# Kernel tuning notes

Hardware: AMD Instinct MI355X
Metric: run time of the kernel (lower is better)

## Reference

```python
import jax, jax.numpy as jnp
import numpy as np

N = 2048      # num_nodes
B = 16        # batch
D_IN = 2      # input_dim per node
UNITS = 64    # rnn_units
F = D_IN + UNITS   # concat feature size = 66
M = 3         # num_matrices = (1 support + 1 adp hop)*K(=1) + 1 identity
E = N * 16    # sparse support edges (avg degree 16)


def _spmm(rows, cols, vals, x):
    # sparse support @ x, x: (N, K); equivalent of torch.sparse.mm
    return jax.ops.segment_sum(vals[:, None] * x[cols], rows, num_segments=N)


def _gconv(inputs, state, W, support_rows, support_cols, support_vals, adp):
    # inputs: (B, N*D_IN), state: (B, N*units) -> out: (B, N*out_dim)
    x = jnp.concatenate([inputs.reshape(B, N, -1), state.reshape(B, N, -1)], axis=2)  # (B,N,F)
    f = x.shape[2]
    x0 = x.transpose(1, 2, 0).reshape(N, f * B)                # (N, F*B)
    # diffusion step 1 over the single random_walk support
    x1 = _spmm(support_rows, support_cols, support_vals, x0)   # (N, F*B)
    # adaptive adjacency, k_hop=1 -> adp_lst = [adp], applied to x0
    x_temp = x0.reshape(N, f, B).transpose(2, 0, 1)            # (B,N,F)
    x2 = jnp.einsum('bnm,bmf->bnf', adp, x_temp)               # (B,N,F)
    x2 = x2.transpose(1, 2, 0).reshape(N, f * B)
    xs = jnp.stack([x0, x1, x2], axis=0)                       # (M,N,F*B)
    xs = xs.reshape(M, N, f, B).transpose(3, 1, 2, 0).reshape(B * N, f * M)
    out = xs @ W                                               # (B*N, out_dim)  (no bias: source never adds it)
    return out.reshape(B, N * W.shape[1])


def setup_inputs() -> dict:
    key = jax.random.key(0)
    ks = jax.random.split(key, 8)
    inputs = jax.random.normal(ks[0], (B, N * D_IN), dtype=jnp.float32)
    hx = jax.random.normal(ks[1], (B, N * UNITS), dtype=jnp.float32)
    adp = jax.random.uniform(ks[2], (B, N, N), dtype=jnp.float32) / N  # ~row-stochastic adaptive adj
    support_rows = jax.random.randint(ks[3], (E,), 0, N, dtype=jnp.int32)
    support_cols = jax.random.randint(ks[4], (E,), 0, N, dtype=jnp.int32)
    support_vals = jax.random.uniform(ks[5], (E,), dtype=jnp.float32) / 16.0
    W_ru = jax.random.normal(ks[6], (F * M, 2 * UNITS), dtype=jnp.float32) * 0.05
    W_c = jax.random.normal(ks[7], (F * M, UNITS), dtype=jnp.float32) * 0.05
    return dict(inputs=inputs, hx=hx, adp=adp, support_rows=support_rows,
                support_cols=support_cols, support_vals=support_vals,
                W_ru=W_ru, W_c=W_c, time_axis=0)


def reference(inputs, hx, adp, support_rows, support_cols, support_vals, W_ru, W_c, time_axis):
    # GRU with graph convolution gates (use_gc_for_ru=True, activation=tanh)
    ru = jax.nn.sigmoid(_gconv(inputs, hx, W_ru, support_rows, support_cols, support_vals, adp))
    ru = ru.reshape(B, N, 2 * UNITS)
    r = ru[..., :UNITS].reshape(B, N * UNITS)
    u = ru[..., UNITS:].reshape(B, N * UNITS)
    c = jnp.tanh(_gconv(inputs, r * hx, W_c, support_rows, support_cols, support_vals, adp))
    return u * hx + (1.0 - u) * c
```

## Files before the change

kernel.cpp:

```cpp
#include <hip/hip_runtime.h>
#include <cstdint>
#include <cstddef>

#define DN 2048
#define DB 16
#define DE 32768
#define FPAD 96

typedef __bf16 bf16x8 __attribute__((ext_vector_type(8)));
typedef float f32x4 __attribute__((ext_vector_type(4)));

__global__ __launch_bounds__(256) void prep_kernel(
    const float* __restrict__ inputs, const float* __restrict__ hx,
    const float* __restrict__ Wru, const float* __restrict__ Wc,
    __bf16* __restrict__ xcat1, __bf16* __restrict__ xcat2,
    __bf16* __restrict__ wtru, __bf16* __restrict__ wtc,
    int* __restrict__ cnt) {
  int idx = blockIdx.x * 256 + threadIdx.x;
  const int T1 = DB * DN * FPAD;
  if (idx < 2 * T1) {
    int which = idx >= T1 ? 1 : 0;
    int i = idx - which * T1;
    int f = i % FPAD;
    int bn = i / FPAD;
    int n = bn & (DN - 1);
    int b = bn >> 11;
    __bf16 v = (__bf16)0.0f;
    if (f < 2) v = (__bf16)inputs[(b << 12) + n * 2 + f];
    else if (f < 66 && !which) v = (__bf16)hx[((size_t)b << 17) + (n << 6) + (f - 2)];
    if (which) xcat2[i] = v; else xcat1[i] = v;
  } else {
    int j = idx - 2 * T1;
    if (j < 384 * FPAD) {
      int k = j % FPAD, o = j / FPAD;
      wtru[j] = (k < 66) ? (__bf16)Wru[(k * 3 + (o >> 7)) * 128 + (o & 127)] : (__bf16)0.0f;
    } else {
      j -= 384 * FPAD;
      if (j < 192 * FPAD) {
        int k = j % FPAD, o = j / FPAD;
        wtc[j] = (k < 66) ? (__bf16)Wc[(k * 3 + (o >> 6)) * 64 + (o & 63)] : (__bf16)0.0f;
      } else {
        j -= 192 * FPAD;
        if (j < DN) cnt[j] = 0;
      }
    }
  }
}

__global__ __launch_bounds__(512) void csr_count(const int* __restrict__ rows,
                                                 int* __restrict__ cnt) {
  int e = blockIdx.x * 512 + threadIdx.x;
  atomicAdd(&cnt[rows[e]], 1);
}

__global__ __launch_bounds__(1024) void csr_scan(const int* __restrict__ cnt,
                                                 int* __restrict__ csr_ptr,
                                                 int* __restrict__ off) {
  __shared__ int sa[DN];
  __shared__ int sb[DN];
  int t = threadIdx.x;
  int c0 = cnt[t], c1 = cnt[t + 1024];
  sa[t] = c0; sa[t + 1024] = c1;
  __syncthreads();
  int* src = sa; int* dst = sb;
  for (int o = 1; o < DN; o <<= 1) {
    for (int i = t; i < DN; i += 1024) {
      int v = src[i];
      if (i >= o) v += src[i - o];
      dst[i] = v;
    }
    __syncthreads();
    int* tmp = src; src = dst; dst = tmp;
  }
  int e0 = src[t] - c0;
  int e1 = src[t + 1024] - c1;
  csr_ptr[t] = e0; csr_ptr[t + 1024] = e1;
  off[t] = e0; off[t + 1024] = e1;
  if (t == 0) csr_ptr[DN] = DE;
}

__global__ __launch_bounds__(512) void csr_scatter(
    const int* __restrict__ rows, const int* __restrict__ cols,
    const float* __restrict__ vals, int* __restrict__ off,
    int* __restrict__ csr_col, float* __restrict__ csr_val) {
  int e = blockIdx.x * 512 + threadIdx.x;
  int r = rows[e];
  int p = atomicAdd(&off[r], 1);
  csr_col[p] = cols[e];
  csr_val[p] = vals[e];
}

template <int OD>
__global__ __launch_bounds__(256) void small_gemm(
    const __bf16* __restrict__ A, const __bf16* __restrict__ Bt,
    float* __restrict__ Y0, __bf16* __restrict__ y1b, __bf16* __restrict__ y2b) {
  __shared__ __attribute__((aligned(16))) __bf16 As[128 * 104];
  __shared__ __attribute__((aligned(16))) __bf16 Bs[64 * 104];
  int tid = threadIdx.x;
  int wave = tid >> 6, lane = tid & 63;
  int lrow = lane & 15, quad = lane >> 4;
  int r0 = blockIdx.x * 128;
  int c0 = blockIdx.y * 64;
  const uint4* gA = (const uint4*)(A + (size_t)r0 * FPAD);
  const uint4* gB = (const uint4*)(Bt + (size_t)c0 * FPAD);
  uint4* sA = (uint4*)As;
  uint4* sB = (uint4*)Bs;
#pragma unroll
  for (int i = 0; i < 6; ++i) {
    int s = i * 256 + tid;
    int r = s / 12, c4 = s % 12;
    sA[r * 13 + c4] = gA[r * 12 + c4];
  }
#pragma unroll
  for (int i = 0; i < 3; ++i) {
    int s = i * 256 + tid;
    int r = s / 12, c4 = s % 12;
    sB[r * 13 + c4] = gB[r * 12 + c4];
  }
  __syncthreads();
  int wm = wave >> 1, wn = wave & 1;
  f32x4 acc[4][2];
#pragma unroll
  for (int mt = 0; mt < 4; ++mt)
#pragma unroll
    for (int nt = 0; nt < 2; ++nt) acc[mt][nt] = (f32x4){0.f, 0.f, 0.f, 0.f};
#pragma unroll
  for (int kk = 0; kk < 3; ++kk) {
    bf16x8 af[4], bv[2];
#pragma unroll
    for (int mt = 0; mt < 4; ++mt)
      af[mt] = *(const bf16x8*)(As + (wm * 64 + mt * 16 + lrow) * 104 + kk * 32 + quad * 8);
#pragma unroll
    for (int nt = 0; nt < 2; ++nt)
      bv[nt] = *(const bf16x8*)(Bs + (wn * 32 + nt * 16 + lrow) * 104 + kk * 32 + quad * 8);
#pragma unroll
    for (int mt = 0; mt < 4; ++mt)
#pragma unroll
      for (int nt = 0; nt < 2; ++nt)
        acc[mt][nt] = __builtin_amdgcn_mfma_f32_16x16x32_bf16(af[mt], bv[nt], acc[mt][nt], 0, 0, 0);
  }
#pragma unroll
  for (int mt = 0; mt < 4; ++mt)
#pragma unroll
    for (int nt = 0; nt < 2; ++nt)
#pragma unroll
      for (int r = 0; r < 4; ++r) {
        int row = r0 + wm * 64 + mt * 16 + quad * 4 + r;
        int col = c0 + wn * 32 + nt * 16 + lrow;
        float v = acc[mt][nt][r];
        int g = col >> ((OD == 128) ? 7 : 6);
        int oo = col & (OD - 1);
        size_t oi = (size_t)row * OD + oo;
        if (g == 0) Y0[oi] = v;
        else if (g == 1) y1b[oi] = (__bf16)v;
        else y2b[oi] = (__bf16)v;
      }
}

template <int OD>
__global__ __launch_bounds__(256) void gather_pre(
    float* __restrict__ Y0, const __bf16* __restrict__ y1b,
    const int* __restrict__ csr_ptr, const int* __restrict__ csr_col,
    const float* __restrict__ csr_val) {
  constexpr int SH = (OD == 128) ? 7 : 6;
  int idx = blockIdx.x * 256 + threadIdx.x;
  int o = idx & (OD - 1);
  int bn = idx >> SH;
  int n = bn & (DN - 1);
  int b = bn >> 11;
  float acc = Y0[idx];
  int e1 = csr_ptr[n + 1];
  const __bf16* yb = y1b + ((size_t)b << 11) * OD;
  for (int e = csr_ptr[n]; e < e1; ++e)
    acc += csr_val[e] * (float)yb[(size_t)csr_col[e] * OD + o];
  Y0[idx] = acc;
}

template <int OD>
__global__ void transpose_y2(const __bf16* __restrict__ y2b, __bf16* __restrict__ y2t) {
  __shared__ __bf16 tile[32][33];
  int b = blockIdx.z;
  int mb = blockIdx.x * 32, ob = blockIdx.y * 32;
  int tx = threadIdx.x, ty = threadIdx.y;
#pragma unroll
  for (int i = 0; i < 4; ++i)
    tile[ty + i * 8][tx] = y2b[(size_t)(b * DN + mb + ty + i * 8) * OD + ob + tx];
  __syncthreads();
#pragma unroll
  for (int i = 0; i < 4; ++i)
    y2t[(size_t)(b * OD + ob + ty + i * 8) * DN + mb + tx] = tile[tx][ty + i * 8];
}

template <int OD, bool IS_RU>
__global__ __launch_bounds__(256, 4) void adp_gemm(
    const float* __restrict__ adp, const __bf16* __restrict__ y2t,
    const float* __restrict__ pre, const float* __restrict__ hx,
    float* __restrict__ u_buf, __bf16* __restrict__ xcat2,
    float* __restrict__ outp) {
  constexpr int BM = 32;
  constexpr int NT = OD / 32;
  constexpr int LDK = 72;
  constexpr int ASZ = BM * LDK;
  __shared__ __attribute__((aligned(16))) __bf16 As[2 * ASZ];
  int tid = threadIdx.x;
  int wave = tid >> 6, lane = tid & 63;
  int lrow = lane & 15, quad = lane >> 4;
  int hw = blockIdx.x;
  int swz = (hw & 7) * 128 + (hw >> 3);
  int b = swz >> 6;
  int row0 = (swz & 63) * BM;
  const float* Ab = adp + ((size_t)b * DN + row0) * DN;
  const __bf16* Bb = y2t + (size_t)b * OD * (size_t)DN;
  int wm = wave >> 1, wn = wave & 1;
  f32x4 acc[NT];
#pragma unroll
  for (int nt = 0; nt < NT; ++nt) acc[nt] = (f32x4){0.f, 0.f, 0.f, 0.f};

  int ar = tid >> 3;
  int ac = (tid & 7) * 8;
  const float* ap = Ab + (size_t)ar * DN + ac;
  int awofs = ar * LDK + ac;
  int arofs = (wm * 16 + lrow) * LDK;

  f32x4 raA0 = *(const f32x4*)ap;
  f32x4 raA1 = *(const f32x4*)(ap + 4);
  f32x4 raB0 = *(const f32x4*)(ap + 64);
  f32x4 raB1 = *(const f32x4*)(ap + 68);

#pragma unroll 1
  for (int c2 = 0; c2 < DN / 128; ++c2) {
    {
      int c = 2 * c2;
      bf16x8 cv;
#pragma unroll
      for (int j = 0; j < 4; ++j) { cv[j] = (__bf16)raA0[j]; cv[4 + j] = (__bf16)raA1[j]; }
      *(bf16x8*)(As + awofs) = cv;
      bf16x8 bv[2][NT];
#pragma unroll
      for (int kk = 0; kk < 2; ++kk)
#pragma unroll
        for (int nt = 0; nt < NT; ++nt) {
          int rb = wn * (NT * 16) + nt * 16 + lrow;
          bv[kk][nt] = *(const bf16x8*)(Bb + (size_t)rb * DN + c * 64 + (kk * 4 + quad) * 8);
        }
      if (c + 2 < DN / 64) {
        const float* pn = ap + (c + 2) * 64;
        raA0 = *(const f32x4*)pn;
        raA1 = *(const f32x4*)(pn + 4);
      }
      __syncthreads();
#pragma unroll
      for (int kk = 0; kk < 2; ++kk) {
        bf16x8 af = *(const bf16x8*)(As + arofs + (kk * 4 + quad) * 8);
#pragma unroll
        for (int nt = 0; nt < NT; ++nt)
          acc[nt] = __builtin_amdgcn_mfma_f32_16x16x32_bf16(af, bv[kk][nt], acc[nt], 0, 0, 0);
      }
    }
    {
      int c = 2 * c2 + 1;
      bf16x8 cv;
#pragma unroll
      for (int j = 0; j < 4; ++j) { cv[j] = (__bf16)raB0[j]; cv[4 + j] = (__bf16)raB1[j]; }
      *(bf16x8*)(As + ASZ + awofs) = cv;
      bf16x8 bv[2][NT];
#pragma unroll
      for (int kk = 0; kk < 2; ++kk)
#pragma unroll
        for (int nt = 0; nt < NT; ++nt) {
          int rb = wn * (NT * 16) + nt * 16 + lrow;
          bv[kk][nt] = *(const bf16x8*)(Bb + (size_t)rb * DN + c * 64 + (kk * 4 + quad) * 8);
        }
      if (c + 2 < DN / 64) {
        const float* pn = ap + (c + 2) * 64;
        raB0 = *(const f32x4*)pn;
        raB1 = *(const f32x4*)(pn + 4);
      }
      __syncthreads();
#pragma unroll
      for (int kk = 0; kk < 2; ++kk) {
        bf16x8 af = *(const bf16x8*)(As + ASZ + arofs + (kk * 4 + quad) * 8);
#pragma unroll
        for (int nt = 0; nt < NT; ++nt)
          acc[nt] = __builtin_amdgcn_mfma_f32_16x16x32_bf16(af, bv[kk][nt], acc[nt], 0, 0, 0);
      }
    }
  }
#pragma unroll
  for (int nt = 0; nt < NT; ++nt)
#pragma unroll
    for (int r = 0; r < 4; ++r) {
      int n = row0 + wm * 16 + quad * 4 + r;
      int o = wn * (NT * 16) + nt * 16 + lrow;
      float g = acc[nt][r] + pre[((size_t)b * DN + n) * OD + o];
      if (IS_RU) {
        float s = 1.f / (1.f + __expf(-g));
        if (o < 64) {
          float hxv = hx[((size_t)b << 17) + n * 64 + o];
          xcat2[((size_t)b * DN + n) * FPAD + 2 + o] = (__bf16)(s * hxv);
        } else {
          u_buf[((size_t)b * DN + n) * 64 + (o - 64)] = s;
        }
      } else {
        float cval = 1.f - 2.f / (__expf(2.f * g) + 1.f);
        float u = u_buf[((size_t)b * DN + n) * 64 + o];
        float hxv = hx[((size_t)b << 17) + n * 64 + o];
        outp[((size_t)b << 17) + n * 64 + o] = u * hxv + (1.f - u) * cval;
      }
    }
}

extern "C" void kernel_launch(void* const* d_in, const int* in_sizes, int n_in,
                              void* d_out, int out_size, void* d_ws, size_t ws_size,
                              hipStream_t stream) {
  const float* inputs = (const float*)d_in[0];
  const float* hx     = (const float*)d_in[1];
  const float* adp    = (const float*)d_in[2];
  const int* srows    = (const int*)d_in[3];
  const int* scols    = (const int*)d_in[4];
  const float* svals  = (const float*)d_in[5];
  const float* Wru    = (const float*)d_in[6];
  const float* Wc     = (const float*)d_in[7];
  float* outp = (float*)d_out;

  char* w = (char*)d_ws;
  auto carve = [&](size_t bytes) -> char* {
    char* p = w;
    w += (bytes + 255) & ~(size_t)255;
    return p;
  };
  int*    csr_ptr = (int*)   carve((DN + 1) * sizeof(int));
  int*    csr_col = (int*)   carve(DE * sizeof(int));
  float*  csr_val = (float*) carve(DE * sizeof(float));
  int*    cnt     = (int*)   carve(DN * sizeof(int));
  int*    off     = (int*)   carve(DN * sizeof(int));
  __bf16* xcat1   = (__bf16*)carve((size_t)DB * DN * FPAD * 2);
  __bf16* xcat2   = (__bf16*)carve((size_t)DB * DN * FPAD * 2);
  __bf16* wtru    = (__bf16*)carve(384 * FPAD * 2);
  __bf16* wtc     = (__bf16*)carve(192 * FPAD * 2);
  float*  Y0      = (float*) carve((size_t)DB * DN * 128 * 4);
  __bf16* y1b     = (__bf16*)carve((size_t)DB * DN * 128 * 2);
  __bf16* y2b     = (__bf16*)carve((size_t)DB * DN * 128 * 2);
  __bf16* y2t     = (__bf16*)carve((size_t)DB * DN * 128 * 2);
  float*  u_buf   = (float*) carve((size_t)DB * DN * 64 * 4);
  (void)ws_size; (void)in_sizes; (void)n_in; (void)out_size;

  prep_kernel<<<24800, 256, 0, stream>>>(inputs, hx, Wru, Wc, xcat1, xcat2,
                                         wtru, wtc, cnt);
  csr_count<<<64, 512, 0, stream>>>(srows, cnt);
  csr_scan<<<1, 1024, 0, stream>>>(cnt, csr_ptr, off);
  csr_scatter<<<64, 512, 0, stream>>>(srows, scols, svals, off, csr_col, csr_val);

  small_gemm<128><<<dim3(256, 6), 256, 0, stream>>>(xcat1, wtru, Y0, y1b, y2b);
  gather_pre<128><<<16384, 256, 0, stream>>>(Y0, y1b, csr_ptr, csr_col, csr_val);
  transpose_y2<128><<<dim3(64, 4, 16), dim3(32, 8), 0, stream>>>(y2b, y2t);
  adp_gemm<128, true><<<1024, 256, 0, stream>>>(
      adp, y2t, Y0, hx, u_buf, xcat2, outp);

  small_gemm<64><<<dim3(256, 3), 256, 0, stream>>>(xcat2, wtc, Y0, y1b, y2b);
  gather_pre<64><<<8192, 256, 0, stream>>>(Y0, y1b, csr_ptr, csr_col, csr_val);
  transpose_y2<64><<<dim3(64, 2, 16), dim3(32, 8), 0, stream>>>(y2b, y2t);
  adp_gemm<64, false><<<1024, 256, 0, stream>>>(
      adp, y2t, Y0, hx, u_buf, xcat2, outp);
}
```

Baseline: 732.0 us.

## Load adp A-fragments directly into registers, dropping LDS staging and barriers

The adaptive-adjacency GEMM no longer stages fp32 adp tiles through shared memory. Each lane now loads its own MFMA A-fragment straight from global memory into registers, converts it to bf16 in registers, and prefetches two k-chunks ahead. This removes the LDS write and read and the __syncthreads per k-step. In exchange, the two waves that share a row block (wn=0,1) now each read the same adp rows, which doubles A-side global/L2 traffic, and the per-lane access pattern is less coalesced.

```diff
diff --git a/kernel.cpp b/kernel.cpp
--- a/kernel.cpp
+++ b/kernel.cpp
@@ -197,95 +197,87 @@
     const float* __restrict__ pre, const float* __restrict__ hx,
     float* __restrict__ u_buf, __bf16* __restrict__ xcat2,
     float* __restrict__ outp) {
-  constexpr int BM = 32;
   constexpr int NT = OD / 32;
-  constexpr int LDK = 72;
-  constexpr int ASZ = BM * LDK;
-  __shared__ __attribute__((aligned(16))) __bf16 As[2 * ASZ];
   int tid = threadIdx.x;
   int wave = tid >> 6, lane = tid & 63;
   int lrow = lane & 15, quad = lane >> 4;
   int hw = blockIdx.x;
   int swz = (hw & 7) * 128 + (hw >> 3);
   int b = swz >> 6;
-  int row0 = (swz & 63) * BM;
-  const float* Ab = adp + ((size_t)b * DN + row0) * DN;
-  const __bf16* Bb = y2t + (size_t)b * OD * (size_t)DN;
+  int row0 = (swz & 63) * 32;
   int wm = wave >> 1, wn = wave & 1;
+  int arow = row0 + wm * 16 + lrow;
+  const float* Ap = adp + ((size_t)b * DN + arow) * DN + quad * 8;
+  const __bf16* Bb = y2t + (size_t)b * OD * (size_t)DN + quad * 8;
+  const __bf16* Bp[NT];
+#pragma unroll
+  for (int nt = 0; nt < NT; ++nt)
+    Bp[nt] = Bb + (size_t)(wn * (NT * 16) + nt * 16 + lrow) * DN;
+
   f32x4 acc[NT];
 #pragma unroll
   for (int nt = 0; nt < NT; ++nt) acc[nt] = (f32x4){0.f, 0.f, 0.f, 0.f};
 
-  int ar = tid >> 3;
-  int ac = (tid & 7) * 8;
-  const float* ap = Ab + (size_t)ar * DN + ac;
-  int awofs = ar * LDK + ac;
-  int arofs = (wm * 16 + lrow) * LDK;
-
-  f32x4 raA0 = *(const f32x4*)ap;
-  f32x4 raA1 = *(const f32x4*)(ap + 4);
-  f32x4 raB0 = *(const f32x4*)(ap + 64);
-  f32x4 raB1 = *(const f32x4*)(ap + 68);
+  f32x4 aE0, aE1, aE2, aE3, aO0, aO1, aO2, aO3;
+#define LOADA(c, a0, a1, a2, a3)                 \
+  {                                              \
+    const float* p_ = Ap + (size_t)(c) * 64;     \
+    a0 = *(const f32x4*)p_;                      \
+    a1 = *(const f32x4*)(p_ + 4);                \
+    a2 = *(const f32x4*)(p_ + 32);               \
+    a3 = *(const f32x4*)(p_ + 36);               \
+  }
+
+  LOADA(0, aE0, aE1, aE2, aE3);
+  LOADA(1, aO0, aO1, aO2, aO3);
 
 #pragma unroll 1
-  for (int c2 = 0; c2 < DN / 128; ++c2) {
+  for (int c = 0; c < DN / 64; c += 2) {
     {
-      int c = 2 * c2;
-      bf16x8 cv;
-#pragma unroll
-      for (int j = 0; j < 4; ++j) { cv[j] = (__bf16)raA0[j]; cv[4 + j] = (__bf16)raA1[j]; }
-      *(bf16x8*)(As + awofs) = cv;
       bf16x8 bv[2][NT];
 #pragma unroll
       for (int kk = 0; kk < 2; ++kk)
 #pragma unroll
-        for (int nt = 0; nt < NT; ++nt) {
-          int rb = wn * (NT * 16) + nt * 16 + lrow;
-          bv[kk][nt] = *(const bf16x8*)(Bb + (size_t)rb * DN + c * 64 + (kk * 4 + quad) * 8);
-        }
-      if (c + 2 < DN / 64) {
-        const float* pn = ap + (c + 2) * 64;
-        raA0 = *(const f32x4*)pn;
-        raA1 = *(const f32x4*)(pn + 4);
-      }
-      __syncthreads();
-#pragma unroll
-      for (int kk = 0; kk < 2; ++kk) {
-        bf16x8 af = *(const bf16x8*)(As + arofs + (kk * 4 + quad) * 8);
-#pragma unroll
         for (int nt = 0; nt < NT; ++nt)
-          acc[nt] = __builtin_amdgcn_mfma_f32_16x16x32_bf16(af, bv[kk][nt], acc[nt], 0, 0, 0);
-      }
+          bv[kk][nt] = *(const bf16x8*)(Bp[nt] + c * 64 + kk * 32);
+      bf16x8 af0, af1;
+#pragma unroll
+      for (int j = 0; j < 4; ++j) {
+        af0[j] = (__bf16)aE0[j]; af0[4 + j] = (__bf16)aE1[j];
+        af1[j] = (__bf16)aE2[j]; af1[4 + j] = (__bf16)aE3[j];
+      }
+      if (c + 2 < DN / 64) LOADA(c + 2, aE0, aE1, aE2, aE3);
+#pragma unroll
+      for (int nt = 0; nt < NT; ++nt)
+        acc[nt] = __builtin_amdgcn_mfma_f32_16x16x32_bf16(af0, bv[0][nt], acc[nt], 0, 0, 0);
+#pragma unroll
+      for (int nt = 0; nt < NT; ++nt)
+        acc[nt] = __builtin_amdgcn_mfma_f32_16x16x32_bf16(af1, bv[1][nt], acc[nt], 0, 0, 0);
     }
     {
-      int c = 2 * c2 + 1;
-      bf16x8 cv;
-#pragma unroll
-      for (int j = 0; j < 4; ++j) { cv[j] = (__bf16)raB0[j]; cv[4 + j] = (__bf16)raB1[j]; }
-      *(bf16x8*)(As + ASZ + awofs) = cv;
       bf16x8 bv[2][NT];
 #pragma unroll
       for (int kk = 0; kk < 2; ++kk)
 #pragma unroll
-        for (int nt = 0; nt < NT; ++nt) {
-          int rb = wn * (NT * 16) + nt * 16 + lrow;
-          bv[kk][nt] = *(const bf16x8*)(Bb + (size_t)rb * DN + c * 64 + (kk * 4 + quad) * 8);
-        }
-      if (c + 2 < DN / 64) {
-        const float* pn = ap + (c + 2) * 64;
-        raB0 = *(const f32x4*)pn;
-        raB1 = *(const f32x4*)(pn + 4);
-      }
-      __syncthreads();
-#pragma unroll
-      for (int kk = 0; kk < 2; ++kk) {
-        bf16x8 af = *(const bf16x8*)(As + ASZ + arofs + (kk * 4 + quad) * 8);
-#pragma unroll
         for (int nt = 0; nt < NT; ++nt)
-          acc[nt] = __builtin_amdgcn_mfma_f32_16x16x32_bf16(af, bv[kk][nt], acc[nt], 0, 0, 0);
-      }
-    }
-  }
+          bv[kk][nt] = *(const bf16x8*)(Bp[nt] + (c + 1) * 64 + kk * 32);
+      bf16x8 af0, af1;
+#pragma unroll
+      for (int j = 0; j < 4; ++j) {
+        af0[j] = (__bf16)aO0[j]; af0[4 + j] = (__bf16)aO1[j];
+        af1[j] = (__bf16)aO2[j]; af1[4 + j] = (__bf16)aO3[j];
+      }
+      if (c + 3 < DN / 64) LOADA(c + 3, aO0, aO1, aO2, aO3);
+#pragma unroll
+      for (int nt = 0; nt < NT; ++nt)
+        acc[nt] = __builtin_amdgcn_mfma_f32_16x16x32_bf16(af0, bv[0][nt], acc[nt], 0, 0, 0);
+#pragma unroll
+      for (int nt = 0; nt < NT; ++nt)
+        acc[nt] = __builtin_amdgcn_mfma_f32_16x16x32_bf16(af1, bv[1][nt], acc[nt], 0, 0, 0);
+    }
+  }
+#undef LOADA
+
 #pragma unroll
   for (int nt = 0; nt < NT; ++nt)
 #pragma unroll
```

Measured after the change: 796.1 us. 1.09x slower.
